# Kernel tuning notes

Hardware: AMD Instinct MI355X
Metric: run time of the kernel (lower is better)

Reference implementation:

```python
import jax, jax.numpy as jnp
import numpy as np

IN, H, OUT = 128, 256, 128
B, T = 256, 512
EPS = 1e-5


def gru_cell(x, h, w_ih, w_hh, b_ih, b_hh):
    # PyTorch GRUCell: gates ordered (r, z, n)
    gi = x @ w_ih.T + b_ih            # (B, 3H)
    gh = h @ w_hh.T + b_hh            # (B, 3H)
    gi_r, gi_z, gi_n = jnp.split(gi, 3, axis=-1)
    gh_r, gh_z, gh_n = jnp.split(gh, 3, axis=-1)
    r = jax.nn.sigmoid(gi_r + gh_r)
    z = jax.nn.sigmoid(gi_z + gh_z)
    n = jnp.tanh(gi_n + r * gh_n)
    return (1.0 - z) * n + z * h


def setup_inputs() -> dict:
    key = jax.random.key(0)
    ks = jax.random.split(key, 12)
    s_in = 1.0 / np.sqrt(H)
    u = lambda k, shp: jax.random.uniform(k, shp, jnp.float32, -s_in, s_in)
    return {
        "x": jax.random.normal(ks[0], (B, T, IN), jnp.float32),
        "w_ih1": u(ks[1], (3 * H, IN)),
        "w_hh1": u(ks[2], (3 * H, H)),
        "b_ih1": u(ks[3], (3 * H,)),
        "b_hh1": u(ks[4], (3 * H,)),
        "w_ih2": u(ks[5], (3 * H, H)),
        "w_hh2": u(ks[6], (3 * H, H)),
        "b_ih2": u(ks[7], (3 * H,)),
        "b_hh2": u(ks[8], (3 * H,)),
        "gamma": jnp.ones((H,), jnp.float32),
        "beta": jnp.zeros((H,), jnp.float32),
        "fc_w": u(ks[9], (OUT, H)),
        "fc_b": u(ks[10], (OUT,)),
    }


def reference(x, w_ih1, w_hh1, b_ih1, b_hh1, w_ih2, w_hh2, b_ih2, b_hh2,
              gamma, beta, fc_w, fc_b):
    batch = x.shape[0]
    h0 = (jnp.zeros((batch, H), x.dtype), jnp.zeros((batch, H), x.dtype))

    def step(carry, xt):
        h1, h2 = carry
        h1 = gru_cell(xt, h1, w_ih1, w_hh1, b_ih1, b_hh1)
        h2 = gru_cell(h1, h2, w_ih2, w_hh2, b_ih2, b_hh2)
        return (h1, h2), h2

    _, seq_hidden = jax.lax.scan(step, h0, jnp.swapaxes(x, 0, 1))  # (T, B, H)
    seq_hidden = jnp.swapaxes(seq_hidden, 0, 1)                    # (B, T, H)

    # SyncBatchNorm in training mode: batch statistics over (batch*time)
    flat = seq_hidden.reshape(-1, H)
    mean = flat.mean(axis=0)
    var = flat.var(axis=0)  # biased variance, as used for normalization
    normed = (flat - mean) * jax.lax.rsqrt(var + EPS) * gamma + beta

    # Hardtanh(-2, 2), temporal mean, linear projection
    act = jnp.clip(normed, -2.0, 2.0).reshape(batch, -1, H)
    summary = act.mean(axis=1)                                     # (B, H)
    return summary @ fc_w.T + fc_b
```

## Files before the change

kernel.cpp:

```cpp
#include <hip/hip_runtime.h>
#include <stdint.h>

#define TT 512
#define BB 256
#define HH 256
#define II 128
#define OUTD 128
#define EPSV 1e-5f

#define NCL 32
#define RPC 8
#define RD1 32
#define RD2 32
#define HPAD 264
#define SPIN_CAP (1 << 17)

#define P_M1 0
#define P_A  1
#define P_M2 2
#define P_B  3

#define OFF_PROG     0u
#define OFF_BNSUM    1024u
#define OFF_BNSQ     2048u
#define OFF_ZERO_END 3072u
#define OFF_GI1      65536u
#define GI_SLOT      16384u
#define GI1_BYTES    ((unsigned)NCL*RD1*GI_SLOT)
#define OFF_H1R      (OFF_GI1 + GI1_BYTES)
#define H1R_BYTES    ((unsigned)NCL*RD2*4096u)
#define OFF_GI2      (OFF_H1R + H1R_BYTES)
#define GI2_BYTES    ((unsigned)NCL*RD2*GI_SLOT)
#define OFF_H2SEQ    (OFF_GI2 + GI2_BYTES)

typedef short bf16x8 __attribute__((ext_vector_type(8)));
typedef float f32x4  __attribute__((ext_vector_type(4)));
typedef unsigned long long u64;

__device__ __forceinline__ short f2bf(float v) {
    unsigned u = __float_as_uint(v);
    u += 0x7fffu + ((u >> 16) & 1u);
    return (short)(u >> 16);
}
__device__ __forceinline__ float bf2f(short s) {
    return __uint_as_float(((unsigned)(unsigned short)s) << 16);
}
__device__ __forceinline__ float bf2f_lo(unsigned u) { return __uint_as_float(u << 16); }
__device__ __forceinline__ float bf2f_hi(unsigned u) { return __uint_as_float(u & 0xffff0000u); }
__device__ __forceinline__ unsigned pk2bf(float a, float b) {
    return (unsigned)(unsigned short)f2bf(a) | ((unsigned)(unsigned short)f2bf(b) << 16);
}
__device__ __forceinline__ bf16x8 ldfrag_f32(const float* __restrict__ p) {
    const float4* q = (const float4*)p;
    float4 a = q[0], b = q[1];
    bf16x8 f;
    f[0]=f2bf(a.x); f[1]=f2bf(a.y); f[2]=f2bf(a.z); f[3]=f2bf(a.w);
    f[4]=f2bf(b.x); f[5]=f2bf(b.y); f[6]=f2bf(b.z); f[7]=f2bf(b.w);
    return f;
}
__device__ __forceinline__ float sigm_f(float x) {
    float e = __expf(-x);
    return __builtin_amdgcn_rcpf(1.f + e);
}
__device__ __forceinline__ float tanh_f(float x) {
    float ax = fabsf(x);
    float e  = __expf(-2.f * ax);
    float t  = (1.f - e) * __builtin_amdgcn_rcpf(1.f + e);
    return copysignf(t, x);
}
__device__ __forceinline__ void poll_ge(const unsigned* p, int tgt) {
    if (tgt <= 0) return;
    int spins = 0;
    while ((int)__hip_atomic_load((unsigned*)p, __ATOMIC_RELAXED, __HIP_MEMORY_SCOPE_SYSTEM) < tgt) {
        __builtin_amdgcn_s_sleep(2);
        if (++spins > SPIN_CAP) break;
    }
    asm volatile("" ::: "memory");
}
__device__ __forceinline__ void poll2_ge(const unsigned* p1, int t1, const unsigned* p2, int t2) {
    int spins = 0;
    for (;;) {
        int a = (int)__hip_atomic_load((unsigned*)p1, __ATOMIC_RELAXED, __HIP_MEMORY_SCOPE_SYSTEM);
        int b = (int)__hip_atomic_load((unsigned*)p2, __ATOMIC_RELAXED, __HIP_MEMORY_SCOPE_SYSTEM);
        if (a >= t1 && b >= t2) break;
        __builtin_amdgcn_s_sleep(2);
        if (++spins > SPIN_CAP) break;
    }
    asm volatile("" ::: "memory");
}
__device__ __forceinline__ void post_prog(unsigned* p, int v) {
    __hip_atomic_store(p, (unsigned)v, __ATOMIC_RELAXED, __HIP_MEMORY_SCOPE_SYSTEM);
}
__device__ __forceinline__ unsigned ld_u32_coh(const unsigned* p) {
    return __hip_atomic_load((unsigned*)p, __ATOMIC_RELAXED, __HIP_MEMORY_SCOPE_SYSTEM);
}
__device__ __forceinline__ void st_u32_coh(unsigned* p, unsigned v) {
    __hip_atomic_store(p, v, __ATOMIC_RELAXED, __HIP_MEMORY_SCOPE_SYSTEM);
}
__device__ __forceinline__ u64 ld_u64_coh(const u64* p) {
    return __hip_atomic_load((u64*)p, __ATOMIC_RELAXED, __HIP_MEMORY_SCOPE_SYSTEM);
}
__device__ __forceinline__ void st_u64_coh(u64* p, u64 v) {
    __hip_atomic_store(p, v, __ATOMIC_RELAXED, __HIP_MEMORY_SCOPE_SYSTEM);
}
#define CFENCE() asm volatile("" ::: "memory")

__global__ void __launch_bounds__(512, 1)
gru_pipe(const float* __restrict__ x,
         const float* __restrict__ wih1, const float* __restrict__ whh1,
         const float* __restrict__ bih1, const float* __restrict__ bhh1,
         const float* __restrict__ wih2, const float* __restrict__ whh2,
         const float* __restrict__ bih2, const float* __restrict__ bhh2,
         char* __restrict__ ws)
{
    const int tid = threadIdx.x, wave = tid >> 6, lane = tid & 63;
    const int qd = lane >> 4, ln = lane & 15;
    const int stage = blockIdx.x & 3;
    const int cl    = blockIdx.x >> 2;
    const int grow0 = cl * RPC;

    unsigned* prog = (unsigned*)(ws + OFF_PROG) + cl * 4;
    short* h2seq = (short*)(ws + OFF_H2SEQ);

    __shared__ __align__(16) short hb[2][16][HPAD];
    {
        short* z = &hb[0][0][0];
        for (int i = tid; i < 2*16*HPAD; i += 512) z[i] = 0;
    }
    __syncthreads();

    if (stage == 0) {
        bf16x8 Wi[2][3][4]; f32x4 cinit[2][3];
        #pragma unroll
        for (int b2 = 0; b2 < 2; ++b2)
        #pragma unroll
        for (int g = 0; g < 3; ++g) {
            const int grow = g*256 + (wave*2 + b2)*16 + ln;
            #pragma unroll
            for (int kc = 0; kc < 4; ++kc)
                Wi[b2][g][kc] = ldfrag_f32(wih1 + grow*II + kc*32 + qd*8);
            float c0 = bih1[grow] + (g < 2 ? bhh1[grow] : 0.f);
            cinit[b2][g] = f32x4{c0, c0, c0, c0};
        }
        const float* xr = x + (size_t)(grow0 + (ln>>2)*2 + (ln&1)) * (TT*II) + qd*8;
        float4 xp[8];
        #pragma unroll
        for (int kc = 0; kc < 4; ++kc) {
            xp[2*kc]   = *(const float4*)(xr + kc*32);
            xp[2*kc+1] = *(const float4*)(xr + kc*32 + 4);
        }

        for (int t = 0; t < TT; ++t) {
            if ((t & 7) == 0) poll_ge(&prog[P_A], t - 24);
            CFENCE();
            bf16x8 a[4];
            #pragma unroll
            for (int kc = 0; kc < 4; ++kc) {
                float4 u = xp[2*kc], v = xp[2*kc+1];
                bf16x8 f;
                f[0]=f2bf(u.x); f[1]=f2bf(u.y); f[2]=f2bf(u.z); f[3]=f2bf(u.w);
                f[4]=f2bf(v.x); f[5]=f2bf(v.y); f[6]=f2bf(v.z); f[7]=f2bf(v.w);
                a[kc] = f;
            }
            if (t + 1 < TT) {
                const float* xn = xr + (size_t)(t+1)*II;
                #pragma unroll
                for (int kc = 0; kc < 4; ++kc) {
                    xp[2*kc]   = *(const float4*)(xn + kc*32);
                    xp[2*kc+1] = *(const float4*)(xn + kc*32 + 4);
                }
            }
            CFENCE();
            f32x4 acc[2][3];
            #pragma unroll
            for (int b2 = 0; b2 < 2; ++b2)
            #pragma unroll
            for (int g = 0; g < 3; ++g) acc[b2][g] = cinit[b2][g];
            #pragma unroll
            for (int kc = 0; kc < 4; ++kc)
            #pragma unroll
            for (int b2 = 0; b2 < 2; ++b2)
            #pragma unroll
            for (int g = 0; g < 3; ++g)
                acc[b2][g] = __builtin_amdgcn_mfma_f32_16x16x32_bf16(a[kc], Wi[b2][g][kc], acc[b2][g], 0, 0, 0);
            CFENCE();
            char* slot = ws + OFF_GI1 + ((size_t)cl*RD1 + (t & (RD1-1)))*GI_SLOT;
            unsigned* rz = (unsigned*)slot;
            u64* nn = (u64*)(slot + 8192);
            #pragma unroll
            for (int b2 = 0; b2 < 2; ++b2) {
                const int tile = wave*2 + b2;
                st_u32_coh(rz + (tile*2 + 0)*64 + lane, pk2bf(acc[b2][0][0], acc[b2][0][1]));
                st_u32_coh(rz + (tile*2 + 1)*64 + lane, pk2bf(acc[b2][1][0], acc[b2][1][1]));
                union { float f[2]; u64 u; } np;
                np.f[0] = acc[b2][2][0]; np.f[1] = acc[b2][2][1];
                st_u64_coh(nn + tile*64 + lane, np.u);
            }
            if (t & 1) {
                asm volatile("s_waitcnt vmcnt(14)" ::: "memory");
                if (tid == 0) post_prog(&prog[P_M1], t - 1);
            }
            asm volatile("s_waitcnt lgkmcnt(0)" ::: "memory");
            __builtin_amdgcn_sched_barrier(0);
            __builtin_amdgcn_s_barrier();
        }
        asm volatile("s_waitcnt vmcnt(0)" ::: "memory");
        __syncthreads();
        if (tid == 0) post_prog(&prog[P_M1], 1000000);

    } else if (stage == 1) {
        bf16x8 Wh[2][3][8]; float bnn[2];
        #pragma unroll
        for (int b2 = 0; b2 < 2; ++b2) {
            const int colg = (wave*2 + b2)*16 + ln;
            #pragma unroll
            for (int g = 0; g < 3; ++g)
                #pragma unroll
                for (int kc = 0; kc < 8; ++kc)
                    Wh[b2][g][kc] = ldfrag_f32(whh1 + (g*256 + colg)*HH + kc*32 + qd*8);
            bnn[b2] = bhh1[512 + colg];
        }
        float hold[2][2] = {{0.f,0.f},{0.f,0.f}};
        unsigned pr0[2], pz0[2], pr1[2], pz1[2]; u64 pn0[2], pn1[2];
        const int tile0 = wave*2, tile1 = wave*2 + 1;

        poll_ge(&prog[P_M1], 2);
        #pragma unroll
        for (int s = 0; s < 2; ++s) {
            char* slot = ws + OFF_GI1 + ((size_t)cl*RD1 + s)*GI_SLOT;
            const unsigned* rz = (const unsigned*)slot;
            const u64* nn = (const u64*)(slot + 8192);
            pr0[s] = ld_u32_coh(rz + (tile0*2+0)*64 + lane);
            pz0[s] = ld_u32_coh(rz + (tile0*2+1)*64 + lane);
            pn0[s] = ld_u64_coh(nn + tile0*64 + lane);
            pr1[s] = ld_u32_coh(rz + (tile1*2+0)*64 + lane);
            pz1[s] = ld_u32_coh(rz + (tile1*2+1)*64 + lane);
            pn1[s] = ld_u64_coh(nn + tile1*64 + lane);
        }

#define A_STEP(T, P)                                                           \
        {                                                                      \
            if (((T) & 7) == 0) poll2_ge(&prog[P_M1], (T)+10, &prog[P_M2], (T)-24); \
            CFENCE();                                                          \
            f32x4 aR[2], aZ[2], aN[2]; float gn[2][2];                         \
            aR[0] = f32x4{bf2f_lo(pr0[P]), bf2f_hi(pr0[P]), 0.f, 0.f};         \
            aZ[0] = f32x4{bf2f_lo(pz0[P]), bf2f_hi(pz0[P]), 0.f, 0.f};         \
            aR[1] = f32x4{bf2f_lo(pr1[P]), bf2f_hi(pr1[P]), 0.f, 0.f};         \
            aZ[1] = f32x4{bf2f_lo(pz1[P]), bf2f_hi(pz1[P]), 0.f, 0.f};         \
            { union { u64 u; float f[2]; } c;                                  \
              c.u = pn0[P]; gn[0][0]=c.f[0]; gn[0][1]=c.f[1];                  \
              c.u = pn1[P]; gn[1][0]=c.f[0]; gn[1][1]=c.f[1]; }                \
            aN[0] = f32x4{bnn[0], bnn[0], 0.f, 0.f};                           \
            aN[1] = f32x4{bnn[1], bnn[1], 0.f, 0.f};                           \
            if ((T) + 2 < TT) {                 \
                char* slot = ws + OFF_GI1 + ((size_t)cl*RD1 + (((T)+2) & (RD1-1)))*GI_SLOT; \
                const unsigned* rz = (const unsigned*)slot;                    \
                const u64* nn = (const u64*)(slot + 8192);                     \
                pr0[P] = ld_u32_coh(rz + (tile0*2+0)*64 + lane);               \
                pz0[P] = ld_u32_coh(rz + (tile0*2+1)*64 + lane);               \
                pn0[P] = ld_u64_coh(nn + tile0*64 + lane);                     \
                pr1[P] = ld_u32_coh(rz + (tile1*2+0)*64 + lane);               \
                pz1[P] = ld_u32_coh(rz + (tile1*2+1)*64 + lane);               \
                pn1[P] = ld_u64_coh(nn + tile1*64 + lane);                     \
            }                                                                  \
            CFENCE();                                                          \
            const int rb = ((T) + 1) & 1, wb = (T) & 1;                        \
            _Pragma("unroll")                                                  \
            for (int kc = 0; kc < 8; ++kc) {                                   \
                bf16x8 f = *(const bf16x8*)&hb[rb][ln][kc*32 + qd*8];          \
                aR[0] = __builtin_amdgcn_mfma_f32_16x16x32_bf16(f, Wh[0][0][kc], aR[0], 0,0,0); \
                aR[1] = __builtin_amdgcn_mfma_f32_16x16x32_bf16(f, Wh[1][0][kc], aR[1], 0,0,0); \
                aZ[0] = __builtin_amdgcn_mfma_f32_16x16x32_bf16(f, Wh[0][1][kc], aZ[0], 0,0,0); \
                aZ[1] = __builtin_amdgcn_mfma_f32_16x16x32_bf16(f, Wh[1][1][kc], aZ[1], 0,0,0); \
                aN[0] = __builtin_amdgcn_mfma_f32_16x16x32_bf16(f, Wh[0][2][kc], aN[0], 0,0,0); \
                aN[1] = __builtin_amdgcn_mfma_f32_16x16x32_bf16(f, Wh[1][2][kc], aN[1], 0,0,0); \
            }                                                                  \
            CFENCE();                                                          \
            unsigned* h1slot = (unsigned*)(ws + OFF_H1R + ((size_t)cl*RD2 + ((T) & (RD2-1)))*4096u); \
            _Pragma("unroll")                                                  \
            for (int b2 = 0; b2 < 2; ++b2) {                                   \
                const int colg = (wave*2 + b2)*16 + ln;                        \
                unsigned pk = 0;                                               \
                _Pragma("unroll")                                              \
                for (int r = 0; r < 2; ++r) {                                  \
                    float rg = sigm_f(aR[b2][r]);                              \
                    float zg = sigm_f(aZ[b2][r]);                              \
                    float ng = tanh_f(gn[b2][r] + rg * aN[b2][r]);             \
                    float h  = (1.f - zg)*ng + zg*hold[b2][r];                 \
                    hold[b2][r] = h;                                           \
                    short hs = f2bf(h);                                        \
                    hb[wb][qd*4 + r][colg] = hs;                               \
                    pk |= (unsigned)(unsigned short)hs << (16*r);              \
                }                                                              \
                st_u32_coh(h1slot + colg*4 + qd, pk);                          \
            }                                                                  \
            if ((T) & 1) {                                                     \
                asm volatile("s_waitcnt vmcnt(8)" ::: "memory");               \
                if (tid == 0) post_prog(&prog[P_A], (T) - 1);                  \
            }                                                                  \
            asm volatile("s_waitcnt lgkmcnt(0)" ::: "memory");                 \
            __builtin_amdgcn_sched_barrier(0);                                 \
            __builtin_amdgcn_s_barrier();                                      \
        }
        for (int t = 0; t < TT; t += 2) {
            A_STEP(t,   0);
            A_STEP(t+1, 1);
        }
#undef A_STEP
        asm volatile("s_waitcnt vmcnt(0)" ::: "memory");
        __syncthreads();
        if (tid == 0) post_prog(&prog[P_A], 1000000);

    } else if (stage == 2) {
        bf16x8 Wi[2][3][8]; float c0s[2][3];
        #pragma unroll
        for (int b2 = 0; b2 < 2; ++b2)
        #pragma unroll
        for (int g = 0; g < 3; ++g) {
            const int grow = g*256 + (wave*2 + b2)*16 + ln;
            #pragma unroll
            for (int kc = 0; kc < 8; ++kc)
                Wi[b2][g][kc] = ldfrag_f32(wih2 + grow*HH + kc*32 + qd*8);
            c0s[b2][g] = bih2[grow] + (g < 2 ? bhh2[grow] : 0.f);
        }
        const int base = (tid & 1) * 8, pcol = tid >> 1;
        u64 vc[2];

        poll_ge(&prog[P_A], 2);
        {
            const u64* h1s = (const u64*)(ws + OFF_H1R + (size_t)cl*RD2*4096u);
            u64 v = ld_u64_coh(h1s + tid);
            unsigned lo = (unsigned)v, hi = (unsigned)(v >> 32);
            hb[0][base + 0][pcol] = (short)lo;
            hb[0][base + 1][pcol] = (short)(lo >> 16);
            hb[0][base + 4][pcol] = (short)hi;
            hb[0][base + 5][pcol] = (short)(hi >> 16);
        }
        vc[0] = ld_u64_coh((const u64*)(ws + OFF_H1R + ((size_t)cl*RD2 + 1)*4096u) + tid);
        vc[1] = ld_u64_coh((const u64*)(ws + OFF_H1R + ((size_t)cl*RD2 + 2)*4096u) + tid);
        __syncthreads();

#define M2_STEP(U, P)                                                          \
        {                                                                      \
            if (((U) & 7) == 0) poll2_ge(&prog[P_A], (U)+11, &prog[P_B], (U)-24); \
            CFENCE();                                                          \
            if ((U) + 1 < TT) {        \
                unsigned lo = (unsigned)vc[P], hi = (unsigned)(vc[P] >> 32);   \
                hb[((U)+1) & 1][base + 0][pcol] = (short)lo;                   \
                hb[((U)+1) & 1][base + 1][pcol] = (short)(lo >> 16);           \
                hb[((U)+1) & 1][base + 4][pcol] = (short)hi;                   \
                hb[((U)+1) & 1][base + 5][pcol] = (short)(hi >> 16);           \
            }                                                                  \
            if ((U) + 3 < TT)                                                  \
                vc[P] = ld_u64_coh((const u64*)(ws + OFF_H1R + ((size_t)cl*RD2 + (((U)+3) & (RD2-1)))*4096u) + tid); \
            CFENCE();                                                          \
            f32x4 acc[2][3];                                                   \
            _Pragma("unroll")                                                  \
            for (int b2 = 0; b2 < 2; ++b2)                                     \
            _Pragma("unroll")                                                  \
            for (int g = 0; g < 3; ++g) {                                      \
                float c0 = c0s[b2][g];                                         \
                acc[b2][g] = f32x4{c0, c0, c0, c0};                            \
            }                                                                  \
            _Pragma("unroll")                                                  \
            for (int kc = 0; kc < 8; ++kc) {                                   \
                bf16x8 f = *(const bf16x8*)&hb[(U) & 1][ln][kc*32 + qd*8];     \
                _Pragma("unroll")                                              \
                for (int b2 = 0; b2 < 2; ++b2)                                 \
                _Pragma("unroll")                                              \
                for (int g = 0; g < 3; ++g)                                    \
                    acc[b2][g] = __builtin_amdgcn_mfma_f32_16x16x32_bf16(f, Wi[b2][g][kc], acc[b2][g], 0, 0, 0); \
            }                                                                  \
            CFENCE();                                                          \
            char* slot = ws + OFF_GI2 + ((size_t)cl*RD2 + ((U) & (RD2-1)))*GI_SLOT; \
            unsigned* rz = (unsigned*)slot;                                    \
            u64* nn = (u64*)(slot + 8192);                                     \
            _Pragma("unroll")                                                  \
            for (int b2 = 0; b2 < 2; ++b2) {                                   \
                const int tile = wave*2 + b2;                                  \
                st_u32_coh(rz + (tile*2 + 0)*64 + lane, pk2bf(acc[b2][0][0], acc[b2][0][1])); \
                st_u32_coh(rz + (tile*2 + 1)*64 + lane, pk2bf(acc[b2][1][0], acc[b2][1][1])); \
                union { float f[2]; u64 u; } np;                               \
                np.f[0] = acc[b2][2][0]; np.f[1] = acc[b2][2][1];              \
                st_u64_coh(nn + tile*64 + lane, np.u);                         \
            }                                                                  \
            if ((U) & 1) {                                                     \
                asm volatile("s_waitcnt vmcnt(7)" ::: "memory");               \
                if (tid == 0) post_prog(&prog[P_M2], (U) - 1);                 \
            }                                                                  \
            asm volatile("s_waitcnt lgkmcnt(0)" ::: "memory");                 \
            __builtin_amdgcn_sched_barrier(0);                                 \
            __builtin_amdgcn_s_barrier();                                      \
        }
        for (int u = 0; u < TT; u += 2) {
            M2_STEP(u,   0);
            M2_STEP(u+1, 1);
        }
#undef M2_STEP
        asm volatile("s_waitcnt vmcnt(0)" ::: "memory");
        __syncthreads();
        if (tid == 0) post_prog(&prog[P_M2], 1000000);

    } else {
        bf16x8 Wh[2][3][8]; float bnn[2];
        #pragma unroll
        for (int b2 = 0; b2 < 2; ++b2) {
            const int colg = (wave*2 + b2)*16 + ln;
            #pragma unroll
            for (int g = 0; g < 3; ++g)
                #pragma unroll
                for (int kc = 0; kc < 8; ++kc)
                    Wh[b2][g][kc] = ldfrag_f32(whh2 + (g*256 + colg)*HH + kc*32 + qd*8);
            bnn[b2] = bhh2[512 + colg];
        }
        float* bnsum = (float*)(ws + OFF_BNSUM);
        float* bnsq  = (float*)(ws + OFF_BNSQ);
        float hold[2][2] = {{0.f,0.f},{0.f,0.f}};
        float cbs[2] = {0.f, 0.f}, cbq[2] = {0.f, 0.f};
        unsigned pr0[2], pz0[2], pr1[2], pz1[2]; u64 pn0[2], pn1[2];
        const int tile0 = wave*2, tile1 = wave*2 + 1;

        poll_ge(&prog[P_M2], 2);
        #pragma unroll
        for (int s = 0; s < 2; ++s) {
            char* slot = ws + OFF_GI2 + ((size_t)cl*RD2 + s)*GI_SLOT;
            const unsigned* rz = (const unsigned*)slot;
            const u64* nn = (const u64*)(slot + 8192);
            pr0[s] = ld_u32_coh(rz + (tile0*2+0)*64 + lane);
            pz0[s] = ld_u32_coh(rz + (tile0*2+1)*64 + lane);
            pn0[s] = ld_u64_coh(nn + tile0*64 + lane);
            pr1[s] = ld_u32_coh(rz + (tile1*2+0)*64 + lane);
            pz1[s] = ld_u32_coh(rz + (tile1*2+1)*64 + lane);
            pn1[s] = ld_u64_coh(nn + tile1*64 + lane);
        }
        __syncthreads();

#define B_STEP(V, P)                                                           \
        {                                                                      \
            if (((V) & 7) == 0) poll_ge(&prog[P_M2], (V)+10);                  \
            CFENCE();                                                          \
            f32x4 aR[2], aZ[2], aN[2]; float gn[2][2];                         \
            aR[0] = f32x4{bf2f_lo(pr0[P]), bf2f_hi(pr0[P]), 0.f, 0.f};         \
            aZ[0] = f32x4{bf2f_lo(pz0[P]), bf2f_hi(pz0[P]), 0.f, 0.f};         \
            aR[1] = f32x4{bf2f_lo(pr1[P]), bf2f_hi(pr1[P]), 0.f, 0.f};         \
            aZ[1] = f32x4{bf2f_lo(pz1[P]), bf2f_hi(pz1[P]), 0.f, 0.f};         \
            { union { u64 u; float f[2]; } c;                                  \
              c.u = pn0[P]; gn[0][0]=c.f[0]; gn[0][1]=c.f[1];                  \
              c.u = pn1[P]; gn[1][0]=c.f[0]; gn[1][1]=c.f[1]; }                \
            aN[0] = f32x4{bnn[0], bnn[0], 0.f, 0.f};                           \
            aN[1] = f32x4{bnn[1], bnn[1], 0.f, 0.f};                           \
            if ((V) + 2 < TT) {                 \
                char* slot = ws + OFF_GI2 + ((size_t)cl*RD2 + (((V)+2) & (RD2-1)))*GI_SLOT; \
                const unsigned* rz = (const unsigned*)slot;                    \
                const u64* nn = (const u64*)(slot + 8192);                     \
                pr0[P] = ld_u32_coh(rz + (tile0*2+0)*64 + lane);               \
                pz0[P] = ld_u32_coh(rz + (tile0*2+1)*64 + lane);               \
                pn0[P] = ld_u64_coh(nn + tile0*64 + lane);                     \
                pr1[P] = ld_u32_coh(rz + (tile1*2+0)*64 + lane);               \
                pz1[P] = ld_u32_coh(rz + (tile1*2+1)*64 + lane);               \
                pn1[P] = ld_u64_coh(nn + tile1*64 + lane);                     \
            }                                                                  \
            CFENCE();                                                          \
            const int rb = ((V) + 1) & 1, wb = (V) & 1;                        \
            _Pragma("unroll")                                                  \
            for (int kc = 0; kc < 8; ++kc) {                                   \
                bf16x8 f = *(const bf16x8*)&hb[rb][ln][kc*32 + qd*8];          \
                aR[0] = __builtin_amdgcn_mfma_f32_16x16x32_bf16(f, Wh[0][0][kc], aR[0], 0,0,0); \
                aR[1] = __builtin_amdgcn_mfma_f32_16x16x32_bf16(f, Wh[1][0][kc], aR[1], 0,0,0); \
                aZ[0] = __builtin_amdgcn_mfma_f32_16x16x32_bf16(f, Wh[0][1][kc], aZ[0], 0,0,0); \
                aZ[1] = __builtin_amdgcn_mfma_f32_16x16x32_bf16(f, Wh[1][1][kc], aZ[1], 0,0,0); \
                aN[0] = __builtin_amdgcn_mfma_f32_16x16x32_bf16(f, Wh[0][2][kc], aN[0], 0,0,0); \
                aN[1] = __builtin_amdgcn_mfma_f32_16x16x32_bf16(f, Wh[1][2][kc], aN[1], 0,0,0); \
            }                                                                  \
            CFENCE();                                                          \
            _Pragma("unroll")                                                  \
            for (int b2 = 0; b2 < 2; ++b2) {                                   \
                const int colg = (wave*2 + b2)*16 + ln;                        \
                _Pragma("unroll")                                              \
                for (int r = 0; r < 2; ++r) {                                  \
                    float rg = sigm_f(aR[b2][r]);                              \
                    float zg = sigm_f(aZ[b2][r]);                              \
                    float ng = tanh_f(gn[b2][r] + rg * aN[b2][r]);             \
                    float h  = (1.f - zg)*ng + zg*hold[b2][r];                 \
                    hold[b2][r] = h;                                           \
                    cbs[b2] += h; cbq[b2] += h*h;                              \
                    short hs = f2bf(h);                                        \
                    hb[wb][qd*4 + r][colg] = hs;                               \
                    h2seq[((size_t)(V)*BB + grow0 + qd*2 + r)*HH + colg] = hs; \
                }                                                              \
            }                                                                  \
            if (((V) & 1) && tid == 0) post_prog(&prog[P_B], (V) - 1);         \
            asm volatile("s_waitcnt lgkmcnt(0)" ::: "memory");                 \
            __builtin_amdgcn_sched_barrier(0);                                 \
            __builtin_amdgcn_s_barrier();                                      \
        }
        for (int v = 0; v < TT; v += 2) {
            B_STEP(v,   0);
            B_STEP(v+1, 1);
        }
#undef B_STEP
        #pragma unroll
        for (int b2 = 0; b2 < 2; ++b2) {
            const int colg = (wave*2 + b2)*16 + ln;
            atomicAdd(&bnsum[colg], cbs[b2]);
            atomicAdd(&bnsq[colg],  cbq[b2]);
        }
        __syncthreads();
        if (tid == 0) post_prog(&prog[P_B], 1000000);
    }
}

__global__ void gru_final(const char* __restrict__ ws,
                          const float* __restrict__ gamma, const float* __restrict__ beta,
                          const float* __restrict__ fcw, const float* __restrict__ fcb,
                          float* __restrict__ out)
{
    __shared__ float summ[HH];
    const int b = blockIdx.x, c = threadIdx.x;
    const float* bnsum = (const float*)(ws + OFF_BNSUM);
    const float* bnsq  = (const float*)(ws + OFF_BNSQ);
    const short* h2seq = (const short*)(ws + OFF_H2SEQ);

    const float inv = 1.f / (float)(BB * TT);
    float mean = bnsum[c] * inv;
    float var  = bnsq[c] * inv - mean * mean;
    float scale = rsqrtf(var + EPSV) * gamma[c];
    float shift = beta[c] - mean * scale;

    const short* p = h2seq + (size_t)b*HH + c;
    float acc = 0.f;
    #pragma unroll 4
    for (int t = 0; t < TT; ++t) {
        float v = bf2f(p[(size_t)t*BB*HH]) * scale + shift;
        v = fminf(fmaxf(v, -2.f), 2.f);
        acc += v;
    }
    summ[c] = acc * (1.f / TT);
    __syncthreads();
    if (c < OUTD) {
        float d = fcb[c];
        const float* wr = fcw + c*HH;
        #pragma unroll 8
        for (int h = 0; h < HH; ++h) d += wr[h] * summ[h];
        out[b*OUTD + c] = d;
    }
}

extern "C" void kernel_launch(void* const* d_in, const int* in_sizes, int n_in,
                              void* d_out, int out_size, void* d_ws, size_t ws_size,
                              hipStream_t stream)
{
    const float* x    = (const float*)d_in[0];
    const float* wih1 = (const float*)d_in[1];
    const float* whh1 = (const float*)d_in[2];
    const float* bih1 = (const float*)d_in[3];
    const float* bhh1 = (const float*)d_in[4];
    const float* wih2 = (const float*)d_in[5];
    const float* whh2 = (const float*)d_in[6];
    const float* bih2 = (const float*)d_in[7];
    const float* bhh2 = (const float*)d_in[8];
    const float* gamma= (const float*)d_in[9];
    const float* beta = (const float*)d_in[10];
    const float* fcw  = (const float*)d_in[11];
    const float* fcb  = (const float*)d_in[12];
    char* ws = (char*)d_ws;

    (void)hipMemsetAsync(ws, 0, OFF_ZERO_END, stream);

    hipLaunchKernelGGL(gru_pipe, dim3(NCL*4), dim3(512), 0, stream,
                       x, wih1, whh1, bih1, bhh1, wih2, whh2, bih2, bhh2, ws);

    hipLaunchKernelGGL(gru_final, dim3(BB), dim3(HH), 0, stream,
                       (const char*)ws, gamma, beta, fcw, fcb, (float*)d_out);
}
```

Measured before the change: 2.006 ms.

## Deepen cross-stage prefetch to four steps and pack gate stores into 64-bit words

Each pipeline stage now prefetches its inputs (x rows or gate slots) four timesteps ahead instead of one or two, unrolling the loops by four with rotating register buffers. The r/z gate stores are packed into single 64-bit coherent stores with a per-tile slot layout, which cuts the number of memory ops per step. Progress posting moves to every step with a lag of five, controlled by explicit vmcnt waits. The aim is to hide coherent-memory latency between the producer and consumer blocks. The cost is more register pressure and a tighter reliance on the waitcnt-based ordering being correct.

```diff
diff --git a/kernel.cpp b/kernel.cpp
--- a/kernel.cpp
+++ b/kernel.cpp
@@ -10,8 +10,7 @@
 
 #define NCL 32
 #define RPC 8
-#define RD1 32
-#define RD2 32
+#define RD  32
 #define HPAD 264
 #define SPIN_CAP (1 << 17)
 
@@ -26,11 +25,11 @@
 #define OFF_ZERO_END 3072u
 #define OFF_GI1      65536u
 #define GI_SLOT      16384u
-#define GI1_BYTES    ((unsigned)NCL*RD1*GI_SLOT)
+#define GI1_BYTES    ((unsigned)NCL*RD*GI_SLOT)
 #define OFF_H1R      (OFF_GI1 + GI1_BYTES)
-#define H1R_BYTES    ((unsigned)NCL*RD2*4096u)
+#define H1R_BYTES    ((unsigned)NCL*RD*4096u)
 #define OFF_GI2      (OFF_H1R + H1R_BYTES)
-#define GI2_BYTES    ((unsigned)NCL*RD2*GI_SLOT)
+#define GI2_BYTES    ((unsigned)NCL*RD*GI_SLOT)
 #define OFF_H2SEQ    (OFF_GI2 + GI2_BYTES)
 
 typedef short bf16x8 __attribute__((ext_vector_type(8)));
@@ -91,19 +90,20 @@
 __device__ __forceinline__ void post_prog(unsigned* p, int v) {
     __hip_atomic_store(p, (unsigned)v, __ATOMIC_RELAXED, __HIP_MEMORY_SCOPE_SYSTEM);
 }
-__device__ __forceinline__ unsigned ld_u32_coh(const unsigned* p) {
-    return __hip_atomic_load((unsigned*)p, __ATOMIC_RELAXED, __HIP_MEMORY_SCOPE_SYSTEM);
+__device__ __forceinline__ u64 ld_u64_coh(const u64* p) {
+    return __hip_atomic_load((u64*)p, __ATOMIC_RELAXED, __HIP_MEMORY_SCOPE_SYSTEM);
+}
+__device__ __forceinline__ void st_u64_coh(u64* p, u64 v) {
+    __hip_atomic_store(p, v, __ATOMIC_RELAXED, __HIP_MEMORY_SCOPE_SYSTEM);
 }
 __device__ __forceinline__ void st_u32_coh(unsigned* p, unsigned v) {
     __hip_atomic_store(p, v, __ATOMIC_RELAXED, __HIP_MEMORY_SCOPE_SYSTEM);
 }
-__device__ __forceinline__ u64 ld_u64_coh(const u64* p) {
-    return __hip_atomic_load((u64*)p, __ATOMIC_RELAXED, __HIP_MEMORY_SCOPE_SYSTEM);
-}
-__device__ __forceinline__ void st_u64_coh(u64* p, u64 v) {
-    __hip_atomic_store(p, v, __ATOMIC_RELAXED, __HIP_MEMORY_SCOPE_SYSTEM);
-}
 #define CFENCE() asm volatile("" ::: "memory")
+#define WAITV(n)  asm volatile("s_waitcnt vmcnt(" #n ")" ::: "memory")
+#define WAITV0()  asm volatile("s_waitcnt vmcnt(0)" ::: "memory")
+#define WAITL0()  asm volatile("s_waitcnt lgkmcnt(0)" ::: "memory")
+#define ENDBAR()  do { __builtin_amdgcn_sched_barrier(0); __builtin_amdgcn_s_barrier(); } while (0)
 
 __global__ void __launch_bounds__(512, 1)
 gru_pipe(const float* __restrict__ x,
@@ -118,6 +118,7 @@
     const int stage = blockIdx.x & 3;
     const int cl    = blockIdx.x >> 2;
     const int grow0 = cl * RPC;
+    const int tile0 = wave*2, tile1 = wave*2 + 1;
 
     unsigned* prog = (unsigned*)(ws + OFF_PROG) + cl * 4;
     short* h2seq = (short*)(ws + OFF_H2SEQ);
@@ -143,68 +144,78 @@
             cinit[b2][g] = f32x4{c0, c0, c0, c0};
         }
         const float* xr = x + (size_t)(grow0 + (ln>>2)*2 + (ln&1)) * (TT*II) + qd*8;
-        float4 xp[8];
-        #pragma unroll
-        for (int kc = 0; kc < 4; ++kc) {
-            xp[2*kc]   = *(const float4*)(xr + kc*32);
-            xp[2*kc+1] = *(const float4*)(xr + kc*32 + 4);
-        }
-
-        for (int t = 0; t < TT; ++t) {
-            if ((t & 7) == 0) poll_ge(&prog[P_A], t - 24);
-            CFENCE();
-            bf16x8 a[4];
-            #pragma unroll
-            for (int kc = 0; kc < 4; ++kc) {
-                float4 u = xp[2*kc], v = xp[2*kc+1];
-                bf16x8 f;
-                f[0]=f2bf(u.x); f[1]=f2bf(u.y); f[2]=f2bf(u.z); f[3]=f2bf(u.w);
-                f[4]=f2bf(v.x); f[5]=f2bf(v.y); f[6]=f2bf(v.z); f[7]=f2bf(v.w);
-                a[kc] = f;
-            }
-            if (t + 1 < TT) {
-                const float* xn = xr + (size_t)(t+1)*II;
-                #pragma unroll
-                for (int kc = 0; kc < 4; ++kc) {
-                    xp[2*kc]   = *(const float4*)(xn + kc*32);
-                    xp[2*kc+1] = *(const float4*)(xn + kc*32 + 4);
-                }
-            }
-            CFENCE();
-            f32x4 acc[2][3];
-            #pragma unroll
-            for (int b2 = 0; b2 < 2; ++b2)
-            #pragma unroll
-            for (int g = 0; g < 3; ++g) acc[b2][g] = cinit[b2][g];
-            #pragma unroll
-            for (int kc = 0; kc < 4; ++kc)
-            #pragma unroll
-            for (int b2 = 0; b2 < 2; ++b2)
-            #pragma unroll
-            for (int g = 0; g < 3; ++g)
-                acc[b2][g] = __builtin_amdgcn_mfma_f32_16x16x32_bf16(a[kc], Wi[b2][g][kc], acc[b2][g], 0, 0, 0);
-            CFENCE();
-            char* slot = ws + OFF_GI1 + ((size_t)cl*RD1 + (t & (RD1-1)))*GI_SLOT;
-            unsigned* rz = (unsigned*)slot;
-            u64* nn = (u64*)(slot + 8192);
-            #pragma unroll
-            for (int b2 = 0; b2 < 2; ++b2) {
-                const int tile = wave*2 + b2;
-                st_u32_coh(rz + (tile*2 + 0)*64 + lane, pk2bf(acc[b2][0][0], acc[b2][0][1]));
-                st_u32_coh(rz + (tile*2 + 1)*64 + lane, pk2bf(acc[b2][1][0], acc[b2][1][1]));
-                union { float f[2]; u64 u; } np;
-                np.f[0] = acc[b2][2][0]; np.f[1] = acc[b2][2][1];
-                st_u64_coh(nn + tile*64 + lane, np.u);
-            }
-            if (t & 1) {
-                asm volatile("s_waitcnt vmcnt(14)" ::: "memory");
-                if (tid == 0) post_prog(&prog[P_M1], t - 1);
-            }
-            asm volatile("s_waitcnt lgkmcnt(0)" ::: "memory");
-            __builtin_amdgcn_sched_barrier(0);
-            __builtin_amdgcn_s_barrier();
-        }
-        asm volatile("s_waitcnt vmcnt(0)" ::: "memory");
+        float4 xf0[8], xf1[8], xf2[8], xf3[8];
+
+#define M1_PRO(S) { const float* xp = xr + (size_t)(S)*II;                     \
+        _Pragma("unroll")                                                      \
+        for (int kc = 0; kc < 4; ++kc) {                                       \
+            xf##S[2*kc]   = *(const float4*)(xp + kc*32);                      \
+            xf##S[2*kc+1] = *(const float4*)(xp + kc*32 + 4);                   \
+        } }
+        M1_PRO(0) M1_PRO(1) M1_PRO(2) M1_PRO(3)
+#undef M1_PRO
+        WAITV0();
+
+#define M1_BODY(T, S)                                                          \
+        {                                                                      \
+            if (tid == 0 && (T) >= 5) post_prog(&prog[P_M1], (T) - 5);         \
+            if (((T) & 7) == 0) poll_ge(&prog[P_A], (T) - 24);                 \
+            CFENCE();                                                          \
+            bf16x8 a[4];                                                       \
+            _Pragma("unroll")                                                  \
+            for (int kc = 0; kc < 4; ++kc) {                                   \
+                float4 u = xf##S[2*kc], v = xf##S[2*kc+1];                     \
+                bf16x8 f;                                                      \
+                f[0]=f2bf(u.x); f[1]=f2bf(u.y); f[2]=f2bf(u.z); f[3]=f2bf(u.w);\
+                f[4]=f2bf(v.x); f[5]=f2bf(v.y); f[6]=f2bf(v.z); f[7]=f2bf(v.w);\
+                a[kc] = f;                                                     \
+            }                                                                  \
+            if ((T) + 4 < TT) {                                                \
+                const float* xn = xr + (size_t)((T)+4)*II;                     \
+                _Pragma("unroll")                                              \
+                for (int kc = 0; kc < 4; ++kc) {                               \
+                    xf##S[2*kc]   = *(const float4*)(xn + kc*32);              \
+                    xf##S[2*kc+1] = *(const float4*)(xn + kc*32 + 4);          \
+                }                                                              \
+            }                                                                  \
+            CFENCE();                                                          \
+            f32x4 acc[2][3];                                                   \
+            _Pragma("unroll")                                                  \
+            for (int b2 = 0; b2 < 2; ++b2)                                     \
+            _Pragma("unroll")                                                  \
+            for (int g = 0; g < 3; ++g) acc[b2][g] = cinit[b2][g];             \
+            _Pragma("unroll")                                                  \
+            for (int kc = 0; kc < 4; ++kc)                                     \
+            _Pragma("unroll")                                                  \
+            for (int b2 = 0; b2 < 2; ++b2)                                     \
+            _Pragma("unroll")                                                  \
+            for (int g = 0; g < 3; ++g)                                        \
+                acc[b2][g] = __builtin_amdgcn_mfma_f32_16x16x32_bf16(a[kc], Wi[b2][g][kc], acc[b2][g], 0, 0, 0); \
+            CFENCE();                                                          \
+            char* slot = ws + OFF_GI1 + ((size_t)cl*RD + ((T) & (RD-1)))*GI_SLOT; \
+            {                                                                  \
+                u64* t0p = (u64*)(slot + tile0*1024);                          \
+                u64 rz = (u64)pk2bf(acc[0][0][0], acc[0][0][1])                \
+                       | ((u64)pk2bf(acc[0][1][0], acc[0][1][1]) << 32);       \
+                st_u64_coh(t0p + lane, rz);                                    \
+                union { float f[2]; u64 u; } np;                               \
+                np.f[0] = acc[0][2][0]; np.f[1] = acc[0][2][1];                \
+                st_u64_coh(t0p + 64 + lane, np.u);                             \
+                u64* t1p = (u64*)(slot + tile1*1024);                          \
+                rz = (u64)pk2bf(acc[1][0][0], acc[1][0][1])                    \
+                   | ((u64)pk2bf(acc[1][1][0], acc[1][1][1]) << 32);           \
+                st_u64_coh(t1p + lane, rz);                                    \
+                np.f[0] = acc[1][2][0]; np.f[1] = acc[1][2][1];                \
+                st_u64_coh(t1p + 64 + lane, np.u);                             \
+            }                                                                  \
+            if ((T) >= TT - 8) { WAITV0(); } else { WAITV(36); }               \
+            ENDBAR();                                                          \
+        }
+        for (int tb = 0; tb < TT; tb += 4) {
+            M1_BODY(tb+0, 0) M1_BODY(tb+1, 1) M1_BODY(tb+2, 2) M1_BODY(tb+3, 3)
+        }
+#undef M1_BODY
+        WAITV0();
         __syncthreads();
         if (tid == 0) post_prog(&prog[P_M1], 1000000);
 
@@ -221,47 +232,43 @@
             bnn[b2] = bhh1[512 + colg];
         }
         float hold[2][2] = {{0.f,0.f},{0.f,0.f}};
-        unsigned pr0[2], pz0[2], pr1[2], pz1[2]; u64 pn0[2], pn1[2];
-        const int tile0 = wave*2, tile1 = wave*2 + 1;
-
-        poll_ge(&prog[P_M1], 2);
-        #pragma unroll
-        for (int s = 0; s < 2; ++s) {
-            char* slot = ws + OFF_GI1 + ((size_t)cl*RD1 + s)*GI_SLOT;
-            const unsigned* rz = (const unsigned*)slot;
-            const u64* nn = (const u64*)(slot + 8192);
-            pr0[s] = ld_u32_coh(rz + (tile0*2+0)*64 + lane);
-            pz0[s] = ld_u32_coh(rz + (tile0*2+1)*64 + lane);
-            pn0[s] = ld_u64_coh(nn + tile0*64 + lane);
-            pr1[s] = ld_u32_coh(rz + (tile1*2+0)*64 + lane);
-            pz1[s] = ld_u32_coh(rz + (tile1*2+1)*64 + lane);
-            pn1[s] = ld_u64_coh(nn + tile1*64 + lane);
-        }
-
-#define A_STEP(T, P)                                                           \
+        u64 prz0[2], pn0[2], prz1[2], pn1[2], prz2[2], pn2[2], prz3[2], pn3[2];
+
+        poll_ge(&prog[P_M1], 3);
+#define A_PRO(S) { char* slot = ws + OFF_GI1 + ((size_t)cl*RD + (S))*GI_SLOT;  \
+        const u64* t0p = (const u64*)(slot + tile0*1024);                      \
+        const u64* t1p = (const u64*)(slot + tile1*1024);                      \
+        prz##S[0] = ld_u64_coh(t0p + lane); pn##S[0] = ld_u64_coh(t0p + 64 + lane); \
+        prz##S[1] = ld_u64_coh(t1p + lane); pn##S[1] = ld_u64_coh(t1p + 64 + lane); }
+        A_PRO(0) A_PRO(1) A_PRO(2) A_PRO(3)
+#undef A_PRO
+        WAITV0();
+
+#define A_BODY(T, S)                                                           \
         {                                                                      \
-            if (((T) & 7) == 0) poll2_ge(&prog[P_M1], (T)+10, &prog[P_M2], (T)-24); \
+            if (tid == 0 && (T) >= 5) post_prog(&prog[P_A], (T) - 5);          \
+            if (((T) & 7) == 0) poll2_ge(&prog[P_M1], (T) + 12, &prog[P_M2], (T) - 24); \
             CFENCE();                                                          \
             f32x4 aR[2], aZ[2], aN[2]; float gn[2][2];                         \
-            aR[0] = f32x4{bf2f_lo(pr0[P]), bf2f_hi(pr0[P]), 0.f, 0.f};         \
-            aZ[0] = f32x4{bf2f_lo(pz0[P]), bf2f_hi(pz0[P]), 0.f, 0.f};         \
-            aR[1] = f32x4{bf2f_lo(pr1[P]), bf2f_hi(pr1[P]), 0.f, 0.f};         \
-            aZ[1] = f32x4{bf2f_lo(pz1[P]), bf2f_hi(pz1[P]), 0.f, 0.f};         \
-            { union { u64 u; float f[2]; } c;                                  \
-              c.u = pn0[P]; gn[0][0]=c.f[0]; gn[0][1]=c.f[1];                  \
-              c.u = pn1[P]; gn[1][0]=c.f[0]; gn[1][1]=c.f[1]; }                \
-            aN[0] = f32x4{bnn[0], bnn[0], 0.f, 0.f};                           \
-            aN[1] = f32x4{bnn[1], bnn[1], 0.f, 0.f};                           \
-            if ((T) + 2 < TT) {                 \
-                char* slot = ws + OFF_GI1 + ((size_t)cl*RD1 + (((T)+2) & (RD1-1)))*GI_SLOT; \
-                const unsigned* rz = (const unsigned*)slot;                    \
-                const u64* nn = (const u64*)(slot + 8192);                     \
-                pr0[P] = ld_u32_coh(rz + (tile0*2+0)*64 + lane);               \
-                pz0[P] = ld_u32_coh(rz + (tile0*2+1)*64 + lane);               \
-                pn0[P] = ld_u64_coh(nn + tile0*64 + lane);                     \
-                pr1[P] = ld_u32_coh(rz + (tile1*2+0)*64 + lane);               \
-                pz1[P] = ld_u32_coh(rz + (tile1*2+1)*64 + lane);               \
-                pn1[P] = ld_u64_coh(nn + tile1*64 + lane);                     \
+            {                                                                  \
+                unsigned rzl = (unsigned)prz##S[0], rzh = (unsigned)(prz##S[0] >> 32); \
+                aR[0] = f32x4{bf2f_lo(rzl), bf2f_hi(rzl), 0.f, 0.f};           \
+                aZ[0] = f32x4{bf2f_lo(rzh), bf2f_hi(rzh), 0.f, 0.f};           \
+                rzl = (unsigned)prz##S[1]; rzh = (unsigned)(prz##S[1] >> 32);  \
+                aR[1] = f32x4{bf2f_lo(rzl), bf2f_hi(rzl), 0.f, 0.f};           \
+                aZ[1] = f32x4{bf2f_lo(rzh), bf2f_hi(rzh), 0.f, 0.f};           \
+                union { u64 u; float f[2]; } c;                                \
+                c.u = pn##S[0]; gn[0][0] = c.f[0]; gn[0][1] = c.f[1];          \
+                c.u = pn##S[1]; gn[1][0] = c.f[0]; gn[1][1] = c.f[1];          \
+                aN[0] = f32x4{bnn[0], bnn[0], 0.f, 0.f};                       \
+                aN[1] = f32x4{bnn[1], bnn[1], 0.f, 0.f};                       \
+            }                                                                  \
+            if ((T) + 4 < TT) {                                                \
+                char* slot = ws + OFF_GI1 + ((size_t)cl*RD + (((T)+4) & (RD-1)))*GI_SLOT; \
+                const u64* t0p = (const u64*)(slot + tile0*1024);              \
+                const u64* t1p = (const u64*)(slot + tile1*1024);              \
+                prz##S[0] = ld_u64_coh(t0p + lane); pn##S[0] = ld_u64_coh(t0p + 64 + lane); \
+                prz##S[1] = ld_u64_coh(t1p + lane); pn##S[1] = ld_u64_coh(t1p + 64 + lane); \
             }                                                                  \
             CFENCE();                                                          \
             const int rb = ((T) + 1) & 1, wb = (T) & 1;                        \
@@ -276,7 +283,7 @@
                 aN[1] = __builtin_amdgcn_mfma_f32_16x16x32_bf16(f, Wh[1][2][kc], aN[1], 0,0,0); \
             }                                                                  \
             CFENCE();                                                          \
-            unsigned* h1slot = (unsigned*)(ws + OFF_H1R + ((size_t)cl*RD2 + ((T) & (RD2-1)))*4096u); \
+            unsigned* h1slot = (unsigned*)(ws + OFF_H1R + ((size_t)cl*RD + ((T) & (RD-1)))*4096u); \
             _Pragma("unroll")                                                  \
             for (int b2 = 0; b2 < 2; ++b2) {                                   \
                 const int colg = (wave*2 + b2)*16 + ln;                        \
@@ -294,20 +301,15 @@
                 }                                                              \
                 st_u32_coh(h1slot + colg*4 + qd, pk);                          \
             }                                                                  \
-            if ((T) & 1) {                                                     \
-                asm volatile("s_waitcnt vmcnt(8)" ::: "memory");               \
-                if (tid == 0) post_prog(&prog[P_A], (T) - 1);                  \
-            }                                                                  \
-            asm volatile("s_waitcnt lgkmcnt(0)" ::: "memory");                 \
-            __builtin_amdgcn_sched_barrier(0);                                 \
-            __builtin_amdgcn_s_barrier();                                      \
-        }
-        for (int t = 0; t < TT; t += 2) {
-            A_STEP(t,   0);
-            A_STEP(t+1, 1);
-        }
-#undef A_STEP
-        asm volatile("s_waitcnt vmcnt(0)" ::: "memory");
+            if ((T) >= TT - 8) { WAITV0(); } else { WAITV(18); }               \
+            WAITL0();                                                          \
+            ENDBAR();                                                          \
+        }
+        for (int tb = 0; tb < TT; tb += 4) {
+            A_BODY(tb+0, 0) A_BODY(tb+1, 1) A_BODY(tb+2, 2) A_BODY(tb+3, 3)
+        }
+#undef A_BODY
+        WAITV0();
         __syncthreads();
         if (tid == 0) post_prog(&prog[P_A], 1000000);
 
@@ -324,35 +326,40 @@
             c0s[b2][g] = bih2[grow] + (g < 2 ? bhh2[grow] : 0.f);
         }
         const int base = (tid & 1) * 8, pcol = tid >> 1;
-        u64 vc[2];
-
-        poll_ge(&prog[P_A], 2);
+        u64 vc0, vc1, vc2, vc3;
+
+        poll_ge(&prog[P_A], 4);
         {
-            const u64* h1s = (const u64*)(ws + OFF_H1R + (size_t)cl*RD2*4096u);
+            const u64* h1s = (const u64*)(ws + OFF_H1R + (size_t)cl*RD*4096u);
             u64 v = ld_u64_coh(h1s + tid);
+            WAITV0();
             unsigned lo = (unsigned)v, hi = (unsigned)(v >> 32);
             hb[0][base + 0][pcol] = (short)lo;
             hb[0][base + 1][pcol] = (short)(lo >> 16);
             hb[0][base + 4][pcol] = (short)hi;
             hb[0][base + 5][pcol] = (short)(hi >> 16);
         }
-        vc[0] = ld_u64_coh((const u64*)(ws + OFF_H1R + ((size_t)cl*RD2 + 1)*4096u) + tid);
-        vc[1] = ld_u64_coh((const u64*)(ws + OFF_H1R + ((size_t)cl*RD2 + 2)*4096u) + tid);
+        vc1 = ld_u64_coh((const u64*)(ws + OFF_H1R + ((size_t)cl*RD + 1)*4096u) + tid);
+        vc2 = ld_u64_coh((const u64*)(ws + OFF_H1R + ((size_t)cl*RD + 2)*4096u) + tid);
+        vc3 = ld_u64_coh((const u64*)(ws + OFF_H1R + ((size_t)cl*RD + 3)*4096u) + tid);
+        vc0 = ld_u64_coh((const u64*)(ws + OFF_H1R + ((size_t)cl*RD + 4)*4096u) + tid);
+        WAITV0();
         __syncthreads();
 
-#define M2_STEP(U, P)                                                          \
+#define M2_BODY(U, SN)              \
         {                                                                      \
-            if (((U) & 7) == 0) poll2_ge(&prog[P_A], (U)+11, &prog[P_B], (U)-24); \
+            if (tid == 0 && (U) >= 5) post_prog(&prog[P_M2], (U) - 5);         \
+            if (((U) & 7) == 0) poll2_ge(&prog[P_A], (U) + 12, &prog[P_B], (U) - 24); \
             CFENCE();                                                          \
             if ((U) + 1 < TT) {        \
-                unsigned lo = (unsigned)vc[P], hi = (unsigned)(vc[P] >> 32);   \
+                unsigned lo = (unsigned)vc##SN, hi = (unsigned)(vc##SN >> 32); \
                 hb[((U)+1) & 1][base + 0][pcol] = (short)lo;                   \
                 hb[((U)+1) & 1][base + 1][pcol] = (short)(lo >> 16);           \
                 hb[((U)+1) & 1][base + 4][pcol] = (short)hi;                   \
                 hb[((U)+1) & 1][base + 5][pcol] = (short)(hi >> 16);           \
             }                                                                  \
-            if ((U) + 3 < TT)                                                  \
-                vc[P] = ld_u64_coh((const u64*)(ws + OFF_H1R + ((size_t)cl*RD2 + (((U)+3) & (RD2-1)))*4096u) + tid); \
+            if ((U) + 5 < TT)                                                  \
+                vc##SN = ld_u64_coh((const u64*)(ws + OFF_H1R + ((size_t)cl*RD + (((U)+5) & (RD-1)))*4096u) + tid); \
             CFENCE();                                                          \
             f32x4 acc[2][3];                                                   \
             _Pragma("unroll")                                                  \
@@ -372,32 +379,31 @@
                     acc[b2][g] = __builtin_amdgcn_mfma_f32_16x16x32_bf16(f, Wi[b2][g][kc], acc[b2][g], 0, 0, 0); \
             }                                                                  \
             CFENCE();                                                          \
-            char* slot = ws + OFF_GI2 + ((size_t)cl*RD2 + ((U) & (RD2-1)))*GI_SLOT; \
-            unsigned* rz = (unsigned*)slot;                                    \
-            u64* nn = (u64*)(slot + 8192);                                     \
-            _Pragma("unroll")                                                  \
-            for (int b2 = 0; b2 < 2; ++b2) {                                   \
-                const int tile = wave*2 + b2;                                  \
-                st_u32_coh(rz + (tile*2 + 0)*64 + lane, pk2bf(acc[b2][0][0], acc[b2][0][1])); \
-                st_u32_coh(rz + (tile*2 + 1)*64 + lane, pk2bf(acc[b2][1][0], acc[b2][1][1])); \
+            char* slot = ws + OFF_GI2 + ((size_t)cl*RD + ((U) & (RD-1)))*GI_SLOT; \
+            {                                                                  \
+                u64* t0p = (u64*)(slot + tile0*1024);                          \
+                u64 rz = (u64)pk2bf(acc[0][0][0], acc[0][0][1])                \
+                       | ((u64)pk2bf(acc[0][1][0], acc[0][1][1]) << 32);       \
+                st_u64_coh(t0p + lane, rz);                                    \
                 union { float f[2]; u64 u; } np;                               \
-                np.f[0] = acc[b2][2][0]; np.f[1] = acc[b2][2][1];              \
-                st_u64_coh(nn + tile*64 + lane, np.u);                         \
-            }                                                                  \
-            if ((U) & 1) {                                                     \
-                asm volatile("s_waitcnt vmcnt(7)" ::: "memory");               \
-                if (tid == 0) post_prog(&prog[P_M2], (U) - 1);                 \
-            }                                                                  \
-            asm volatile("s_waitcnt lgkmcnt(0)" ::: "memory");                 \
-            __builtin_amdgcn_sched_barrier(0);                                 \
-            __builtin_amdgcn_s_barrier();                                      \
-        }
-        for (int u = 0; u < TT; u += 2) {
-            M2_STEP(u,   0);
-            M2_STEP(u+1, 1);
-        }
-#undef M2_STEP
-        asm volatile("s_waitcnt vmcnt(0)" ::: "memory");
+                np.f[0] = acc[0][2][0]; np.f[1] = acc[0][2][1];                \
+                st_u64_coh(t0p + 64 + lane, np.u);                             \
+                u64* t1p = (u64*)(slot + tile1*1024);                          \
+                rz = (u64)pk2bf(acc[1][0][0], acc[1][0][1])                    \
+                   | ((u64)pk2bf(acc[1][1][0], acc[1][1][1]) << 32);           \
+                st_u64_coh(t1p + lane, rz);                                    \
+                np.f[0] = acc[1][2][0]; np.f[1] = acc[1][2][1];                \
+                st_u64_coh(t1p + 64 + lane, np.u);                             \
+            }                                                                  \
+            if ((U) >= TT - 8) { WAITV0(); } else { WAITV(15); }               \
+            WAITL0();                                                          \
+            ENDBAR();                                                          \
+        }
+        for (int ub = 0; ub < TT; ub += 4) {
+            M2_BODY(ub+0, 1) M2_BODY(ub+1, 2) M2_BODY(ub+2, 3) M2_BODY(ub+3, 0)
+        }
+#undef M2_BODY
+        WAITV0();
         __syncthreads();
         if (tid == 0) post_prog(&prog[P_M2], 1000000);
 
@@ -417,48 +423,44 @@
         float* bnsq  = (float*)(ws + OFF_BNSQ);
         float hold[2][2] = {{0.f,0.f},{0.f,0.f}};
         float cbs[2] = {0.f, 0.f}, cbq[2] = {0.f, 0.f};
-        unsigned pr0[2], pz0[2], pr1[2], pz1[2]; u64 pn0[2], pn1[2];
-        const int tile0 = wave*2, tile1 = wave*2 + 1;
-
-        poll_ge(&prog[P_M2], 2);
-        #pragma unroll
-        for (int s = 0; s < 2; ++s) {
-            char* slot = ws + OFF_GI2 + ((size_t)cl*RD2 + s)*GI_SLOT;
-            const unsigned* rz = (const unsigned*)slot;
-            const u64* nn = (const u64*)(slot + 8192);
-            pr0[s] = ld_u32_coh(rz + (tile0*2+0)*64 + lane);
-            pz0[s] = ld_u32_coh(rz + (tile0*2+1)*64 + lane);
-            pn0[s] = ld_u64_coh(nn + tile0*64 + lane);
-            pr1[s] = ld_u32_coh(rz + (tile1*2+0)*64 + lane);
-            pz1[s] = ld_u32_coh(rz + (tile1*2+1)*64 + lane);
-            pn1[s] = ld_u64_coh(nn + tile1*64 + lane);
-        }
+        u64 prz0[2], pn0[2], prz1[2], pn1[2], prz2[2], pn2[2], prz3[2], pn3[2];
+
+        poll_ge(&prog[P_M2], 3);
+#define B_PRO(S) { char* slot = ws + OFF_GI2 + ((size_t)cl*RD + (S))*GI_SLOT;  \
+        const u64* t0p = (const u64*)(slot + tile0*1024);                      \
+        const u64* t1p = (const u64*)(slot + tile1*1024);                      \
+        prz##S[0] = ld_u64_coh(t0p + lane); pn##S[0] = ld_u64_coh(t0p + 64 + lane); \
+        prz##S[1] = ld_u64_coh(t1p + lane); pn##S[1] = ld_u64_coh(t1p + 64 + lane); }
+        B_PRO(0) B_PRO(1) B_PRO(2) B_PRO(3)
+#undef B_PRO
+        WAITV0();
         __syncthreads();
 
-#define B_STEP(V, P)                                                           \
+#define B_BODY(V, S)                                                           \
         {                                                                      \
-            if (((V) & 7) == 0) poll_ge(&prog[P_M2], (V)+10);                  \
+            if (tid == 0 && (V) >= 5) post_prog(&prog[P_B], (V) - 5);          \
+            if (((V) & 7) == 0) poll_ge(&prog[P_M2], (V) + 12);                \
             CFENCE();                                                          \
             f32x4 aR[2], aZ[2], aN[2]; float gn[2][2];                         \
-            aR[0] = f32x4{bf2f_lo(pr0[P]), bf2f_hi(pr0[P]), 0.f, 0.f};         \
-            aZ[0] = f32x4{bf2f_lo(pz0[P]), bf2f_hi(pz0[P]), 0.f, 0.f};         \
-            aR[1] = f32x4{bf2f_lo(pr1[P]), bf2f_hi(pr1[P]), 0.f, 0.f};         \
-            aZ[1] = f32x4{bf2f_lo(pz1[P]), bf2f_hi(pz1[P]), 0.f, 0.f};         \
-            { union { u64 u; float f[2]; } c;                                  \
-              c.u = pn0[P]; gn[0][0]=c.f[0]; gn[0][1]=c.f[1];                  \
-              c.u = pn1[P]; gn[1][0]=c.f[0]; gn[1][1]=c.f[1]; }                \
-            aN[0] = f32x4{bnn[0], bnn[0], 0.f, 0.f};                           \
-            aN[1] = f32x4{bnn[1], bnn[1], 0.f, 0.f};                           \
-            if ((V) + 2 < TT) {                 \
-                char* slot = ws + OFF_GI2 + ((size_t)cl*RD2 + (((V)+2) & (RD2-1)))*GI_SLOT; \
-                const unsigned* rz = (const unsigned*)slot;                    \
-                const u64* nn = (const u64*)(slot + 8192);                     \
-                pr0[P] = ld_u32_coh(rz + (tile0*2+0)*64 + lane);               \
-                pz0[P] = ld_u32_coh(rz + (tile0*2+1)*64 + lane);               \
-                pn0[P] = ld_u64_coh(nn + tile0*64 + lane);                     \
-                pr1[P] = ld_u32_coh(rz + (tile1*2+0)*64 + lane);               \
-                pz1[P] = ld_u32_coh(rz + (tile1*2+1)*64 + lane);               \
-                pn1[P] = ld_u64_coh(nn + tile1*64 + lane);                     \
+            {                                                                  \
+                unsigned rzl = (unsigned)prz##S[0], rzh = (unsigned)(prz##S[0] >> 32); \
+                aR[0] = f32x4{bf2f_lo(rzl), bf2f_hi(rzl), 0.f, 0.f};           \
+                aZ[0] = f32x4{bf2f_lo(rzh), bf2f_hi(rzh), 0.f, 0.f};           \
+                rzl = (unsigned)prz##S[1]; rzh = (unsigned)(prz##S[1] >> 32);  \
+                aR[1] = f32x4{bf2f_lo(rzl), bf2f_hi(rzl), 0.f, 0.f};           \
+                aZ[1] = f32x4{bf2f_lo(rzh), bf2f_hi(rzh), 0.f, 0.f};           \
+                union { u64 u; float f[2]; } c;                                \
+                c.u = pn##S[0]; gn[0][0] = c.f[0]; gn[0][1] = c.f[1];          \
+                c.u = pn##S[1]; gn[1][0] = c.f[0]; gn[1][1] = c.f[1];          \
+                aN[0] = f32x4{bnn[0], bnn[0], 0.f, 0.f};                       \
+                aN[1] = f32x4{bnn[1], bnn[1], 0.f, 0.f};                       \
+            }                                                                  \
+            if ((V) + 4 < TT) {                                                \
+                char* slot = ws + OFF_GI2 + ((size_t)cl*RD + (((V)+4) & (RD-1)))*GI_SLOT; \
+                const u64* t0p = (const u64*)(slot + tile0*1024);              \
+                const u64* t1p = (const u64*)(slot + tile1*1024);              \
+                prz##S[0] = ld_u64_coh(t0p + lane); pn##S[0] = ld_u64_coh(t0p + 64 + lane); \
+                prz##S[1] = ld_u64_coh(t1p + lane); pn##S[1] = ld_u64_coh(t1p + 64 + lane); \
             }                                                                  \
             CFENCE();                                                          \
             const int rb = ((V) + 1) & 1, wb = (V) & 1;                        \
@@ -489,22 +491,21 @@
                     h2seq[((size_t)(V)*BB + grow0 + qd*2 + r)*HH + colg] = hs; \
                 }                                                              \
             }                                                                  \
-            if (((V) & 1) && tid == 0) post_prog(&prog[P_B], (V) - 1);         \
-            asm volatile("s_waitcnt lgkmcnt(0)" ::: "memory");                 \
-            __builtin_amdgcn_sched_barrier(0);                                 \
-            __builtin_amdgcn_s_barrier();                                      \
-        }
-        for (int v = 0; v < TT; v += 2) {
-            B_STEP(v,   0);
-            B_STEP(v+1, 1);
-        }
-#undef B_STEP
+            if ((V) >= TT - 8) { WAITV0(); } else { WAITV(24); }               \
+            WAITL0();                                                          \
+            ENDBAR();                                                          \
+        }
+        for (int vb = 0; vb < TT; vb += 4) {
+            B_BODY(vb+0, 0) B_BODY(vb+1, 1) B_BODY(vb+2, 2) B_BODY(vb+3, 3)
+        }
+#undef B_BODY
         #pragma unroll
         for (int b2 = 0; b2 < 2; ++b2) {
             const int colg = (wave*2 + b2)*16 + ln;
             atomicAdd(&bnsum[colg], cbs[b2]);
             atomicAdd(&bnsq[colg],  cbq[b2]);
         }
+        WAITV0();
         __syncthreads();
         if (tid == 0) post_prog(&prog[P_B], 1000000);
     }
```

Result: slower. 3.062 ms (+52.7%).
